# Optimization experiments

Measured on AMD Instinct MI355X. Metric: run time of the kernel, lower is better.

## Reference

```python
import jax, jax.numpy as jnp
import numpy as np

B, C, H, W = 8, 512, 90, 160
CK = C // 8
OUT = 512


def setup_inputs() -> dict:
    key = jax.random.key(0)
    ks = jax.random.split(key, 10)
    s = 0.02
    return {
        "x": jax.random.normal(ks[0], (B, C, H, W), dtype=jnp.float32),
        "Wq": jax.random.normal(ks[1], (CK, C), dtype=jnp.float32) * s,
        "bq": jax.random.normal(ks[2], (CK,), dtype=jnp.float32) * s,
        "Wk": jax.random.normal(ks[3], (CK, C), dtype=jnp.float32) * s,
        "bk": jax.random.normal(ks[4], (CK,), dtype=jnp.float32) * s,
        "Wv": jax.random.normal(ks[5], (C, C), dtype=jnp.float32) * s,
        "bv": jax.random.normal(ks[6], (C,), dtype=jnp.float32) * s,
        "gamma": jax.random.normal(ks[7], (1,), dtype=jnp.float32) * s,
        "Wo": jax.random.normal(ks[8], (OUT, C), dtype=jnp.float32) * s,
        "bo": jax.random.normal(ks[9], (OUT,), dtype=jnp.float32) * s,
    }


def reference(x, Wq, bq, Wk, bk, Wv, bv, gamma, Wo, bo):
    b, c, h, w = x.shape
    n = h * w
    xf = x.reshape(b, c, n)                                   # [B,C,N]
    # 1x1 convs == channel matmuls
    q = jnp.einsum('kc,bcn->bkn', Wq, xf) + bq[None, :, None]  # [B,CK,N]
    k = jnp.einsum('kc,bcn->bkn', Wk, xf) + bk[None, :, None]  # [B,CK,N]
    v = jnp.einsum('oc,bcn->bon', Wv, xf) + bv[None, :, None]  # [B,C,N]
    k = jax.nn.softmax(k, axis=2)   # softmax over spatial
    q = jax.nn.softmax(q, axis=1)   # softmax over channel
    # linear attention: small [CK,C] context, never an NxN map
    context = jnp.einsum('bkn,bcn->bkc', k, v)                 # [B,CK,C]
    out = jnp.einsum('bkc,bkn->bcn', context, q)               # [B,C,N]
    out = gamma[0] * out + xf
    out = jnp.einsum('oc,bcn->bon', Wo, out) + bo[None, :, None]
    return out.reshape(b, -1, h, w)
```

## Files before the change

### kernel.cpp

```cpp
#include <hip/hip_runtime.h>
#include <math.h>

#define NSP   14400
#define CCH   512
#define CKC   64
#define BSZ   8
#define OUTC  512

typedef unsigned short u16;
typedef unsigned int   u32;
typedef __attribute__((ext_vector_type(8))) short bf16x8;
typedef __attribute__((ext_vector_type(4))) float f32x4;

__device__ __forceinline__ u16 f2b(float f) {
    u32 u = __float_as_uint(f);
    return (u16)((u + 0x7fffu + ((u >> 16) & 1u)) >> 16);
}
__device__ __forceinline__ float b2f(u16 h) {
    return __uint_as_float(((u32)h) << 16);
}

__global__ __launch_bounds__(256) void prep_w(
    const float* __restrict__ Wq, const float* __restrict__ Wk,
    const float* __restrict__ Wo, const float* __restrict__ bq,
    const float* __restrict__ bk,
    u16* __restrict__ wqk, u16* __restrict__ wo_bf, float* __restrict__ bqk)
{
    int idx = blockIdx.x * 256 + threadIdx.x;
    if (idx < 128 * 512) {
        int r = idx >> 9, c = idx & 511;
        float v = (r < 64) ? Wq[r * 512 + c] : Wk[(r - 64) * 512 + c];
        wqk[idx] = f2b(v);
    } else if (idx < 128 * 512 + 512 * 512) {
        int i = idx - 128 * 512;
        wo_bf[i] = f2b(Wo[i]);
    } else if (idx < 128 * 512 + 512 * 512 + 128) {
        int i = idx - (128 * 512 + 512 * 512);
        bqk[i] = (i < 64) ? bq[i] : bk[i - 64];
    }
}

__global__ __launch_bounds__(256) void wov_gemm(
    const float* __restrict__ A, const float* __restrict__ B, float* __restrict__ Cg)
{
    const int t = threadIdx.x;
    const int n0 = blockIdx.x * 64, m0 = blockIdx.y * 64;
    __shared__ float As[16][68], Bs[16][68];
    const int ti = t >> 4, tj = t & 15;
    const int a_kk = t & 15, a_mm = t >> 4;
    const int b_nn = t & 63, b_kk = t >> 6;
    float acc[4][4] = {};
    for (int k0 = 0; k0 < 512; k0 += 16) {
        #pragma unroll
        for (int r = 0; r < 4; ++r)
            As[a_kk][a_mm + r * 16] = A[(size_t)(m0 + a_mm + r * 16) * 512 + k0 + a_kk];
        #pragma unroll
        for (int r = 0; r < 4; ++r)
            Bs[b_kk + r * 4][b_nn] = B[(size_t)(k0 + b_kk + r * 4) * 512 + n0 + b_nn];
        __syncthreads();
        #pragma unroll
        for (int kk = 0; kk < 16; ++kk) {
            const float4 a4 = *(const float4*)&As[kk][ti * 4];
            const float4 b4 = *(const float4*)&Bs[kk][tj * 4];
            const float av[4] = {a4.x, a4.y, a4.z, a4.w};
            const float bv[4] = {b4.x, b4.y, b4.z, b4.w};
            #pragma unroll
            for (int i = 0; i < 4; ++i)
                #pragma unroll
                for (int j = 0; j < 4; ++j)
                    acc[i][j] = fmaf(av[i], bv[j], acc[i][j]);
        }
        __syncthreads();
    }
    #pragma unroll
    for (int i = 0; i < 4; ++i) {
        float4 o = {acc[i][0], acc[i][1], acc[i][2], acc[i][3]};
        *(float4*)&Cg[(size_t)(m0 + ti * 4 + i) * 512 + n0 + tj * 4] = o;
    }
}

__global__ __launch_bounds__(64) void bov_kernel(
    const float* __restrict__ Wo, const float* __restrict__ bv, float* __restrict__ bov)
{
    int o = blockIdx.x * 64 + threadIdx.x;
    float s = 0.f;
    for (int c = 0; c < 512; ++c) s += Wo[(size_t)o * 512 + c] * bv[c];
    bov[o] = s;
}

__global__ __launch_bounds__(256) void xpose_cvt(
    const float* __restrict__ x, u16* __restrict__ xT)
{
    const int b = blockIdx.z, c0 = blockIdx.y * 64, n0 = blockIdx.x * 64;
    const int t = threadIdx.x, w = t >> 6;
    __shared__ float T[64][65];
    const float* xp = x + ((size_t)b * CCH + c0) * NSP + n0;
    const int nn = t & 63;
    #pragma unroll
    for (int r = 0; r < 16; ++r) {
        int cc = r * 4 + w;
        T[cc][nn] = xp[(size_t)cc * NSP + nn];
    }
    __syncthreads();
    u16* op = xT + ((size_t)b * NSP + n0) * CCH + c0;
    const int cw = t & 63;
    #pragma unroll
    for (int r = 0; r < 16; ++r) {
        int nr = r * 4 + w;
        op[(size_t)nr * CCH + cw] = f2b(T[cw][nr]);
    }
}

template<int MODE>
__global__ __launch_bounds__(256) void gemm_mfma(
    const u16* __restrict__ A, int lda, long aBatch,
    const u16* __restrict__ Bm, int K, long bBatch,
    float* __restrict__ outF, u16* __restrict__ outH, long cBatch,
    const float* __restrict__ bias, const u16* __restrict__ Ybf, long yBatch)
{
    const int t = threadIdx.x, lane = t & 63, w = t >> 6;
    const int b  = blockIdx.z;
    const int m0 = blockIdx.x * 128;
    const int n0 = blockIdx.y * 96;
    const int wm = w >> 1, wn = w & 1;

    __shared__ __align__(16) u16 As[128 * 64];
    __shared__ __align__(16) u16 Bs[96 * 64];

    const u16* Ap = A + (size_t)b * aBatch;
    const u16* Bp = Bm + (size_t)b * bBatch;

    const int srow = lane >> 3;
    const int kus  = (lane & 7) * 8;

    f32x4 acc[4][3];
    #pragma unroll
    for (int i = 0; i < 4; ++i)
        #pragma unroll
        for (int j = 0; j < 3; ++j)
            acc[i][j] = (f32x4){0.f, 0.f, 0.f, 0.f};

    for (int k0 = 0; k0 < K; k0 += 64) {
        bf16x8 ar[4], br[3];
        #pragma unroll
        for (int i = 0; i < 4; ++i) {
            int row = (w * 4 + i) * 8 + srow;
            ar[i] = *(const bf16x8*)(Ap + (size_t)(m0 + row) * lda + k0 + kus);
        }
        #pragma unroll
        for (int i = 0; i < 3; ++i) {
            int row = (w * 3 + i) * 8 + srow;
            br[i] = *(const bf16x8*)(Bp + (size_t)(n0 + row) * K + k0 + kus);
        }
        __syncthreads();
        #pragma unroll
        for (int i = 0; i < 4; ++i) {
            int row = (w * 4 + i) * 8 + srow;
            *(bf16x8*)&As[row * 64 + (kus ^ ((row & 7) << 3))] = ar[i];
        }
        #pragma unroll
        for (int i = 0; i < 3; ++i) {
            int row = (w * 3 + i) * 8 + srow;
            *(bf16x8*)&Bs[row * 64 + (kus ^ ((row & 7) << 3))] = br[i];
        }
        __syncthreads();
        #pragma unroll
        for (int kk = 0; kk < 2; ++kk) {
            const int kf = kk * 32 + (lane >> 4) * 8;
            bf16x8 af[4], bg[3];
            #pragma unroll
            for (int fm = 0; fm < 4; ++fm) {
                int ml = wm * 64 + fm * 16 + (lane & 15);
                af[fm] = *(const bf16x8*)&As[ml * 64 + (kf ^ ((ml & 7) << 3))];
            }
            #pragma unroll
            for (int fn = 0; fn < 3; ++fn) {
                int nl = wn * 48 + fn * 16 + (lane & 15);
                bg[fn] = *(const bf16x8*)&Bs[nl * 64 + (kf ^ ((nl & 7) << 3))];
            }
            #pragma unroll
            for (int fm = 0; fm < 4; ++fm)
                #pragma unroll
                for (int fn = 0; fn < 3; ++fn)
                    acc[fm][fn] = __builtin_amdgcn_mfma_f32_16x16x32_bf16(
                        af[fm], bg[fn], acc[fm][fn], 0, 0, 0);
        }
    }

    const int rbase = (lane >> 4) * 4;
    const int cloc  = lane & 15;
    #pragma unroll
    for (int fm = 0; fm < 4; ++fm) {
        #pragma unroll
        for (int fn = 0; fn < 3; ++fn) {
            const int gm0 = m0 + wm * 64 + fm * 16 + rbase;
            const int gn  = n0 + wn * 48 + fn * 16 + cloc;
            #pragma unroll
            for (int r = 0; r < 4; ++r) {
                const int gm = gm0 + r;
                const float v = acc[fm][fn][r];
                const size_t idx = (size_t)b * cBatch + (size_t)gm * NSP + gn;
                if (MODE == 0)      outF[idx] = v + bias[gm];
                else if (MODE == 1) outH[idx] = f2b(v + bias[gm]);
                else                outF[idx] = v + b2f(Ybf[(size_t)b * yBatch + (size_t)gm * NSP + gn]);
            }
        }
    }
}

__global__ __launch_bounds__(256) void k_stats(
    const float* __restrict__ Oqk, float* __restrict__ kmax, float* __restrict__ kinv)
{
    const int row = blockIdx.x;
    const int b = row >> 6, k = row & 63;
    const float4* p4 = (const float4*)(Oqk + ((size_t)b * 128 + 64 + k) * NSP);
    const int t = threadIdx.x;

    float m = -1e30f;
    for (int i = t; i < NSP / 4; i += 256) {
        float4 v = p4[i];
        m = fmaxf(m, fmaxf(fmaxf(v.x, v.y), fmaxf(v.z, v.w)));
    }
    for (int o = 32; o; o >>= 1) m = fmaxf(m, __shfl_xor(m, o));
    __shared__ float redm[4];
    const int wid = t >> 6, lane = t & 63;
    if (lane == 0) redm[wid] = m;
    __syncthreads();
    m = fmaxf(fmaxf(redm[0], redm[1]), fmaxf(redm[2], redm[3]));

    float s = 0.f;
    for (int i = t; i < NSP / 4; i += 256) {
        float4 v = p4[i];
        s += __expf(v.x - m) + __expf(v.y - m) + __expf(v.z - m) + __expf(v.w - m);
    }
    for (int o = 32; o; o >>= 1) s += __shfl_xor(s, o);
    __shared__ float reds[4];
    if (lane == 0) reds[wid] = s;
    __syncthreads();
    s = reds[0] + reds[1] + reds[2] + reds[3];
    if (t == 0) { kmax[row] = m; kinv[row] = 1.0f / s; }
}

__global__ __launch_bounds__(256) void q_softmax(
    const float* __restrict__ Oqk, u16* __restrict__ qT)
{
    const long idx = (long)blockIdx.x * 256 + threadIdx.x;
    const int b = (int)(idx / NSP);
    const int n = (int)(idx % NSP);
    const float* base = Oqk + (size_t)b * 128 * NSP + n;
    float q[64];
    float m = -1e30f;
    #pragma unroll
    for (int k = 0; k < 64; ++k) { q[k] = base[(size_t)k * NSP]; m = fmaxf(m, q[k]); }
    float s = 0.f;
    #pragma unroll
    for (int k = 0; k < 64; ++k) { q[k] = __expf(q[k] - m); s += q[k]; }
    const float inv = 1.0f / s;
    u32 pk[32];
    #pragma unroll
    for (int i = 0; i < 32; ++i) {
        pk[i] = (u32)f2b(q[2 * i] * inv) | ((u32)f2b(q[2 * i + 1] * inv) << 16);
    }
    uint4* dst = (uint4*)(qT + ((size_t)b * NSP + n) * 64);
    const uint4* src = (const uint4*)pk;
    #pragma unroll
    for (int i = 0; i < 8; ++i) dst[i] = src[i];
}

__global__ __launch_bounds__(256) void kx_partial(
    const float* __restrict__ Oqk, const float* __restrict__ x,
    const float* __restrict__ kmax, const float* __restrict__ kinv,
    float* __restrict__ part)
{
    const int c0 = blockIdx.x * 64;
    const int sp = blockIdx.y;
    const int b  = blockIdx.z;
    const int t  = threadIdx.x;
    const int ti = t >> 4, tj = t & 15;
    __shared__ float Ks[16][68];
    __shared__ float Vs[16][68];
    const int l_nn = t & 15, l_r0 = t >> 4;
    const float* kbase = Oqk + ((size_t)b * 128 + 64) * NSP;
    const float* xbase = x + (size_t)b * CCH * NSP;

    float km[4], ki[4];
    #pragma unroll
    for (int r = 0; r < 4; ++r) {
        int k = l_r0 + r * 16;
        km[r] = kmax[b * 64 + k];
        ki[r] = kinv[b * 64 + k];
    }
    float acc[4][4] = {};
    const int ns = sp * 960;
    for (int n0 = ns; n0 < ns + 960; n0 += 16) {
        #pragma unroll
        for (int r = 0; r < 4; ++r) {
            int kc = l_r0 + r * 16;
            Ks[l_nn][kc] = __expf(kbase[(size_t)kc * NSP + n0 + l_nn] - km[r]) * ki[r];
            Vs[l_nn][kc] = xbase[(size_t)(c0 + kc) * NSP + n0 + l_nn];
        }
        __syncthreads();
        #pragma unroll
        for (int nn = 0; nn < 16; ++nn) {
            const float4 a4 = *(const float4*)&Ks[nn][ti * 4];
            const float4 b4 = *(const float4*)&Vs[nn][tj * 4];
            const float av[4] = {a4.x, a4.y, a4.z, a4.w};
            const float bv[4] = {b4.x, b4.y, b4.z, b4.w};
            #pragma unroll
            for (int i = 0; i < 4; ++i)
                #pragma unroll
                for (int j = 0; j < 4; ++j)
                    acc[i][j] = fmaf(av[i], bv[j], acc[i][j]);
        }
        __syncthreads();
    }
    #pragma unroll
    for (int i = 0; i < 4; ++i) {
        float4 o = {acc[i][0], acc[i][1], acc[i][2], acc[i][3]};
        *(float4*)&part[(size_t)sp * (BSZ * 64 * 512) +
                        ((size_t)b * 64 + ti * 4 + i) * 512 + c0 + tj * 4] = o;
    }
}

__global__ __launch_bounds__(256) void kx_reduce(
    const float* __restrict__ part, float* __restrict__ KXf)
{
    const size_t idx = (size_t)blockIdx.x * 256 + threadIdx.x;
    float s = 0.f;
    #pragma unroll
    for (int sp = 0; sp < 15; ++sp) s += part[(size_t)sp * 262144 + idx];
    KXf[idx] = s;
}

__global__ __launch_bounds__(256) void wco_gemm(
    const float* __restrict__ Wov, const float* __restrict__ KXf,
    const float* __restrict__ bov, const float* __restrict__ gamma,
    u16* __restrict__ Wco)
{
    const int t = threadIdx.x;
    const int n0 = blockIdx.x * 64, m0 = blockIdx.y * 64;
    __shared__ float As[16][68], Bs[16][68];
    const int ti = t >> 4, tj = t & 15;
    const int a_kk = t & 15, a_mm = t >> 4;
    const int s_nn = t & 63, s_kq = t >> 6;
    float acc[4][4] = {};
    for (int k0 = 0; k0 < 512; k0 += 16) {
        #pragma unroll
        for (int r = 0; r < 4; ++r)
            As[a_kk][a_mm + r * 16] = Wov[(size_t)(m0 + a_mm + r * 16) * 512 + k0 + a_kk];
        {
            const float4 v = *(const float4*)&KXf[(size_t)(n0 + s_nn) * 512 + k0 + s_kq * 4];
            Bs[s_kq * 4 + 0][s_nn] = v.x;
            Bs[s_kq * 4 + 1][s_nn] = v.y;
            Bs[s_kq * 4 + 2][s_nn] = v.z;
            Bs[s_kq * 4 + 3][s_nn] = v.w;
        }
        __syncthreads();
        #pragma unroll
        for (int kk = 0; kk < 16; ++kk) {
            const float4 a4 = *(const float4*)&As[kk][ti * 4];
            const float4 b4 = *(const float4*)&Bs[kk][tj * 4];
            const float av[4] = {a4.x, a4.y, a4.z, a4.w};
            const float bv[4] = {b4.x, b4.y, b4.z, b4.w};
            #pragma unroll
            for (int i = 0; i < 4; ++i)
                #pragma unroll
                for (int j = 0; j < 4; ++j)
                    acc[i][j] = fmaf(av[i], bv[j], acc[i][j]);
        }
        __syncthreads();
    }
    const float g = gamma[0];
    #pragma unroll
    for (int i = 0; i < 4; ++i) {
        const int m = m0 + ti * 4 + i;
        const float bb = bov[m];
        #pragma unroll
        for (int j = 0; j < 4; ++j)
            Wco[(size_t)m * 512 + n0 + tj * 4 + j] = f2b(g * (acc[i][j] + bb));
    }
}

extern "C" void kernel_launch(void* const* d_in, const int* in_sizes, int n_in,
                              void* d_out, int out_size, void* d_ws, size_t ws_size,
                              hipStream_t stream)
{
    const float* x     = (const float*)d_in[0];
    const float* Wq    = (const float*)d_in[1];
    const float* bq    = (const float*)d_in[2];
    const float* Wk    = (const float*)d_in[3];
    const float* bk    = (const float*)d_in[4];
    const float* Wv    = (const float*)d_in[5];
    const float* bv    = (const float*)d_in[6];
    const float* gamma = (const float*)d_in[7];
    const float* Wo    = (const float*)d_in[8];
    const float* bo    = (const float*)d_in[9];
    float* out = (float*)d_out;

    char* base = (char*)d_ws;
    size_t off = 0;
    auto carve = [&](size_t bytes) { char* p = base + off; off = (off + bytes + 255) & ~(size_t)255; return p; };
    u16*   wqk   = (u16*)  carve(128 * 512 * 2);
    u16*   wo_bf = (u16*)  carve(512 * 512 * 2);
    float* bqk   = (float*)carve(128 * 4);
    float* Wov   = (float*)carve(512 * 512 * 4);
    float* bovp  = (float*)carve(512 * 4);
    u16*   xT    = (u16*)  carve((size_t)BSZ * NSP * CCH * 2);
    float* Oqk   = (float*)carve((size_t)BSZ * 128 * NSP * 4);
    u16*   Ybf   = (u16*)  carve((size_t)BSZ * 512 * NSP * 2);
    float* kmax  = (float*)carve(512 * 4);
    float* kinv  = (float*)carve(512 * 4);
    u16*   qT    = (u16*)  carve((size_t)BSZ * NSP * 64 * 2);
    float* part  = (float*)carve((size_t)15 * BSZ * 64 * 512 * 4);
    float* KXf   = (float*)carve((size_t)BSZ * 64 * 512 * 4);
    u16*   Wco   = (u16*)  carve(512 * 512 * 2);

    prep_w<<<dim3((128 * 512 + 512 * 512 + 128 + 255) / 256), dim3(256), 0, stream>>>(
        Wq, Wk, Wo, bq, bk, wqk, wo_bf, bqk);
    wov_gemm<<<dim3(8, 8), dim3(256), 0, stream>>>(Wo, Wv, Wov);
    bov_kernel<<<dim3(8), dim3(64), 0, stream>>>(Wo, bv, bovp);
    xpose_cvt<<<dim3(NSP / 64, CCH / 64, BSZ), dim3(256), 0, stream>>>(x, xT);
    gemm_mfma<0><<<dim3(1, NSP / 96, BSZ), dim3(256), 0, stream>>>(
        wqk, 512, 0L, xT, 512, (long)NSP * 512,
        Oqk, (u16*)nullptr, (long)128 * NSP, bqk, (const u16*)nullptr, 0L);
    gemm_mfma<1><<<dim3(4, NSP / 96, BSZ), dim3(256), 0, stream>>>(
        wo_bf, 512, 0L, xT, 512, (long)NSP * 512,
        (float*)nullptr, Ybf, (long)512 * NSP, bo, (const u16*)nullptr, 0L);
    k_stats<<<dim3(BSZ * 64), dim3(256), 0, stream>>>(Oqk, kmax, kinv);
    q_softmax<<<dim3(BSZ * NSP / 256), dim3(256), 0, stream>>>(Oqk, qT);
    kx_partial<<<dim3(CCH / 64, 15, BSZ), dim3(256), 0, stream>>>(Oqk, x, kmax, kinv, part);
    kx_reduce<<<dim3(262144 / 256), dim3(256), 0, stream>>>(part, KXf);
    wco_gemm<<<dim3(8, 8), dim3(256), 0, stream>>>(Wov, KXf, bovp, gamma, Wco);
    gemm_mfma<2><<<dim3(4, NSP / 96, BSZ), dim3(256), 0, stream>>>(
        Wco, 512, 64L, qT, 64, (long)NSP * 64,
        out, (u16*)nullptr, (long)512 * NSP, (const float*)nullptr, Ybf, (long)512 * NSP);
}
```

Baseline: 858.6 us.

## Fuse q-softmax into QK GEMM, use MFMA for KX, merge output GEMMs

After: 705.4 us. -17.8%, faster.

```diff
diff --git a/kernel.cpp b/kernel.cpp
--- a/kernel.cpp
+++ b/kernel.cpp
@@ -3,9 +3,7 @@
 
 #define NSP   14400
 #define CCH   512
-#define CKC   64
 #define BSZ   8
-#define OUTC  512
 
 typedef unsigned short u16;
 typedef unsigned int   u32;
@@ -15,9 +13,6 @@
 __device__ __forceinline__ u16 f2b(float f) {
     u32 u = __float_as_uint(f);
     return (u16)((u + 0x7fffu + ((u >> 16) & 1u)) >> 16);
-}
-__device__ __forceinline__ float b2f(u16 h) {
-    return __uint_as_float(((u32)h) << 16);
 }
 
 __global__ __launch_bounds__(256) void prep_w(
@@ -89,17 +84,20 @@
 }
 
 __global__ __launch_bounds__(256) void xpose_cvt(
-    const float* __restrict__ x, u16* __restrict__ xT)
+    const float* __restrict__ x, u16* __restrict__ xT, u16* __restrict__ xbf)
 {
     const int b = blockIdx.z, c0 = blockIdx.y * 64, n0 = blockIdx.x * 64;
     const int t = threadIdx.x, w = t >> 6;
     __shared__ float T[64][65];
     const float* xp = x + ((size_t)b * CCH + c0) * NSP + n0;
+    u16* op2 = xbf + ((size_t)b * CCH + c0) * NSP + n0;
     const int nn = t & 63;
     #pragma unroll
     for (int r = 0; r < 16; ++r) {
         int cc = r * 4 + w;
-        T[cc][nn] = xp[(size_t)cc * NSP + nn];
+        float v = xp[(size_t)cc * NSP + nn];
+        T[cc][nn] = v;
+        op2[(size_t)cc * NSP + nn] = f2b(v);
     }
     __syncthreads();
     u16* op = xT + ((size_t)b * NSP + n0) * CCH + c0;
@@ -111,25 +109,20 @@
     }
 }
 
-template<int MODE>
-__global__ __launch_bounds__(256) void gemm_mfma(
-    const u16* __restrict__ A, int lda, long aBatch,
-    const u16* __restrict__ Bm, int K, long bBatch,
-    float* __restrict__ outF, u16* __restrict__ outH, long cBatch,
-    const float* __restrict__ bias, const u16* __restrict__ Ybf, long yBatch)
+__global__ __launch_bounds__(256) void qk_gemm(
+    const u16* __restrict__ wqk, const u16* __restrict__ xT,
+    const float* __restrict__ bqk,
+    float* __restrict__ Okk, u16* __restrict__ qT)
 {
     const int t = threadIdx.x, lane = t & 63, w = t >> 6;
     const int b  = blockIdx.z;
-    const int m0 = blockIdx.x * 128;
-    const int n0 = blockIdx.y * 96;
+    const int n0 = blockIdx.x * 96;
     const int wm = w >> 1, wn = w & 1;
 
     __shared__ __align__(16) u16 As[128 * 64];
     __shared__ __align__(16) u16 Bs[96 * 64];
 
-    const u16* Ap = A + (size_t)b * aBatch;
-    const u16* Bp = Bm + (size_t)b * bBatch;
-
+    const u16* Bp = xT + (size_t)b * NSP * 512;
     const int srow = lane >> 3;
     const int kus  = (lane & 7) * 8;
 
@@ -140,17 +133,17 @@
         for (int j = 0; j < 3; ++j)
             acc[i][j] = (f32x4){0.f, 0.f, 0.f, 0.f};
 
-    for (int k0 = 0; k0 < K; k0 += 64) {
+    for (int k0 = 0; k0 < 512; k0 += 64) {
         bf16x8 ar[4], br[3];
         #pragma unroll
         for (int i = 0; i < 4; ++i) {
             int row = (w * 4 + i) * 8 + srow;
-            ar[i] = *(const bf16x8*)(Ap + (size_t)(m0 + row) * lda + k0 + kus);
+            ar[i] = *(const bf16x8*)(wqk + (size_t)row * 512 + k0 + kus);
         }
         #pragma unroll
         for (int i = 0; i < 3; ++i) {
             int row = (w * 3 + i) * 8 + srow;
-            br[i] = *(const bf16x8*)(Bp + (size_t)(n0 + row) * K + k0 + kus);
+            br[i] = *(const bf16x8*)(Bp + (size_t)(n0 + row) * 512 + k0 + kus);
         }
         __syncthreads();
         #pragma unroll
@@ -189,31 +182,64 @@
 
     const int rbase = (lane >> 4) * 4;
     const int cloc  = lane & 15;
-    #pragma unroll
-    for (int fm = 0; fm < 4; ++fm) {
+    if (wm == 0) {
         #pragma unroll
         for (int fn = 0; fn < 3; ++fn) {
-            const int gm0 = m0 + wm * 64 + fm * 16 + rbase;
-            const int gn  = n0 + wn * 48 + fn * 16 + cloc;
-            #pragma unroll
-            for (int r = 0; r < 4; ++r) {
-                const int gm = gm0 + r;
-                const float v = acc[fm][fn][r];
-                const size_t idx = (size_t)b * cBatch + (size_t)gm * NSP + gn;
-                if (MODE == 0)      outF[idx] = v + bias[gm];
-                else if (MODE == 1) outH[idx] = f2b(v + bias[gm]);
-                else                outF[idx] = v + b2f(Ybf[(size_t)b * yBatch + (size_t)gm * NSP + gn]);
+            const int gn = n0 + wn * 48 + fn * 16 + cloc;
+            float v[4][4];
+            float mx = -1e30f;
+            #pragma unroll
+            for (int fm = 0; fm < 4; ++fm)
+                #pragma unroll
+                for (int r = 0; r < 4; ++r) {
+                    v[fm][r] = acc[fm][fn][r] + bqk[fm * 16 + rbase + r];
+                    mx = fmaxf(mx, v[fm][r]);
+                }
+            mx = fmaxf(mx, __shfl_xor(mx, 16));
+            mx = fmaxf(mx, __shfl_xor(mx, 32));
+            float s = 0.f;
+            #pragma unroll
+            for (int fm = 0; fm < 4; ++fm)
+                #pragma unroll
+                for (int r = 0; r < 4; ++r) {
+                    v[fm][r] = __expf(v[fm][r] - mx);
+                    s += v[fm][r];
+                }
+            s += __shfl_xor(s, 16);
+            s += __shfl_xor(s, 32);
+            const float inv = 1.0f / s;
+            u16* qrow = qT + ((size_t)b * NSP + gn) * 64;
+            #pragma unroll
+            for (int fm = 0; fm < 4; ++fm) {
+                ushort4 pk;
+                pk.x = f2b(v[fm][0] * inv);
+                pk.y = f2b(v[fm][1] * inv);
+                pk.z = f2b(v[fm][2] * inv);
+                pk.w = f2b(v[fm][3] * inv);
+                *(ushort4*)&qrow[fm * 16 + rbase] = pk;
+            }
+        }
+    } else {
+        #pragma unroll
+        for (int fm = 0; fm < 4; ++fm) {
+            #pragma unroll
+            for (int fn = 0; fn < 3; ++fn) {
+                const int gn = n0 + wn * 48 + fn * 16 + cloc;
+                #pragma unroll
+                for (int r = 0; r < 4; ++r) {
+                    const int gmk = fm * 16 + rbase + r;
+                    Okk[((size_t)b * 64 + gmk) * NSP + gn] = acc[fm][fn][r] + bqk[64 + gmk];
+                }
             }
         }
     }
 }
 
 __global__ __launch_bounds__(256) void k_stats(
-    const float* __restrict__ Oqk, float* __restrict__ kmax, float* __restrict__ kinv)
+    const float* __restrict__ Okk, float* __restrict__ kmax, float* __restrict__ kinv)
 {
     const int row = blockIdx.x;
-    const int b = row >> 6, k = row & 63;
-    const float4* p4 = (const float4*)(Oqk + ((size_t)b * 128 + 64 + k) * NSP);
+    const float4* p4 = (const float4*)(Okk + (size_t)row * NSP);
     const int t = threadIdx.x;
 
     float m = -1e30f;
@@ -241,85 +267,108 @@
     if (t == 0) { kmax[row] = m; kinv[row] = 1.0f / s; }
 }
 
-__global__ __launch_bounds__(256) void q_softmax(
-    const float* __restrict__ Oqk, u16* __restrict__ qT)
-{
-    const long idx = (long)blockIdx.x * 256 + threadIdx.x;
-    const int b = (int)(idx / NSP);
-    const int n = (int)(idx % NSP);
-    const float* base = Oqk + (size_t)b * 128 * NSP + n;
-    float q[64];
-    float m = -1e30f;
-    #pragma unroll
-    for (int k = 0; k < 64; ++k) { q[k] = base[(size_t)k * NSP]; m = fmaxf(m, q[k]); }
-    float s = 0.f;
-    #pragma unroll
-    for (int k = 0; k < 64; ++k) { q[k] = __expf(q[k] - m); s += q[k]; }
-    const float inv = 1.0f / s;
-    u32 pk[32];
-    #pragma unroll
-    for (int i = 0; i < 32; ++i) {
-        pk[i] = (u32)f2b(q[2 * i] * inv) | ((u32)f2b(q[2 * i + 1] * inv) << 16);
-    }
-    uint4* dst = (uint4*)(qT + ((size_t)b * NSP + n) * 64);
-    const uint4* src = (const uint4*)pk;
-    #pragma unroll
-    for (int i = 0; i < 8; ++i) dst[i] = src[i];
-}
-
-__global__ __launch_bounds__(256) void kx_partial(
-    const float* __restrict__ Oqk, const float* __restrict__ x,
+__global__ __launch_bounds__(256) void kx_mfma(
+    const float* __restrict__ Okk, const u16* __restrict__ xbf,
     const float* __restrict__ kmax, const float* __restrict__ kinv,
     float* __restrict__ part)
 {
-    const int c0 = blockIdx.x * 64;
-    const int sp = blockIdx.y;
-    const int b  = blockIdx.z;
-    const int t  = threadIdx.x;
-    const int ti = t >> 4, tj = t & 15;
-    __shared__ float Ks[16][68];
-    __shared__ float Vs[16][68];
-    const int l_nn = t & 15, l_r0 = t >> 4;
-    const float* kbase = Oqk + ((size_t)b * 128 + 64) * NSP;
-    const float* xbase = x + (size_t)b * CCH * NSP;
-
-    float km[4], ki[4];
-    #pragma unroll
-    for (int r = 0; r < 4; ++r) {
-        int k = l_r0 + r * 16;
-        km[r] = kmax[b * 64 + k];
-        ki[r] = kinv[b * 64 + k];
-    }
-    float acc[4][4] = {};
-    const int ns = sp * 960;
-    for (int n0 = ns; n0 < ns + 960; n0 += 16) {
-        #pragma unroll
-        for (int r = 0; r < 4; ++r) {
-            int kc = l_r0 + r * 16;
-            Ks[l_nn][kc] = __expf(kbase[(size_t)kc * NSP + n0 + l_nn] - km[r]) * ki[r];
-            Vs[l_nn][kc] = xbase[(size_t)(c0 + kc) * NSP + n0 + l_nn];
-        }
-        __syncthreads();
-        #pragma unroll
-        for (int nn = 0; nn < 16; ++nn) {
-            const float4 a4 = *(const float4*)&Ks[nn][ti * 4];
-            const float4 b4 = *(const float4*)&Vs[nn][tj * 4];
-            const float av[4] = {a4.x, a4.y, a4.z, a4.w};
-            const float bv[4] = {b4.x, b4.y, b4.z, b4.w};
-            #pragma unroll
-            for (int i = 0; i < 4; ++i)
-                #pragma unroll
-                for (int j = 0; j < 4; ++j)
-                    acc[i][j] = fmaf(av[i], bv[j], acc[i][j]);
-        }
-        __syncthreads();
-    }
-    #pragma unroll
-    for (int i = 0; i < 4; ++i) {
-        float4 o = {acc[i][0], acc[i][1], acc[i][2], acc[i][3]};
-        *(float4*)&part[(size_t)sp * (BSZ * 64 * 512) +
-                        ((size_t)b * 64 + ti * 4 + i) * 512 + c0 + tj * 4] = o;
-    }
+    const int bid = blockIdx.x;
+    const int swz = (bid & 7) * 100 + (bid >> 3);
+    const int c_t = swz & 3;
+    const int tmp = swz >> 2;
+    const int sp  = tmp % 25;
+    const int b   = tmp / 25;
+    const int c0  = c_t * 128;
+    const int t = threadIdx.x, lane = t & 63, w = t >> 6;
+
+    __shared__ __align__(16) u16 As[64 * 64];
+    __shared__ __align__(16) u16 Bs[128 * 64];
+    __shared__ float kms[64], kis[64];
+    if (t < 64) { kms[t] = kmax[b * 64 + t]; kis[t] = kinv[b * 64 + t]; }
+    __syncthreads();
+
+    const float* kb = Okk + (size_t)b * 64 * NSP;
+    const u16*   xb = xbf + ((size_t)b * CCH + c0) * NSP;
+
+    const int arow = t >> 4;
+    const int acol = (t & 15) * 4;
+    const int brow = t >> 3;
+    const int bgr  = (t & 7) * 8;
+
+    f32x4 acc[4][2];
+    #pragma unroll
+    for (int i = 0; i < 4; ++i)
+        #pragma unroll
+        for (int j = 0; j < 2; ++j)
+            acc[i][j] = (f32x4){0.f, 0.f, 0.f, 0.f};
+
+    const int ns = sp * 576;
+    for (int nb = ns; nb < ns + 576; nb += 64) {
+        float4 av[4];
+        bf16x8 bv[4];
+        #pragma unroll
+        for (int p = 0; p < 4; ++p) {
+            int row = arow + p * 16;
+            av[p] = *(const float4*)&kb[(size_t)row * NSP + nb + acol];
+        }
+        #pragma unroll
+        for (int p = 0; p < 4; ++p) {
+            int row = brow + p * 32;
+            bv[p] = *(const bf16x8*)&xb[(size_t)row * NSP + nb + bgr];
+        }
+        __syncthreads();
+        #pragma unroll
+        for (int p = 0; p < 4; ++p) {
+            int row = arow + p * 16;
+            float km = kms[row], ki = kis[row];
+            ushort4 e;
+            e.x = f2b(__expf(av[p].x - km) * ki);
+            e.y = f2b(__expf(av[p].y - km) * ki);
+            e.z = f2b(__expf(av[p].z - km) * ki);
+            e.w = f2b(__expf(av[p].w - km) * ki);
+            *(ushort4*)&As[row * 64 + (acol ^ ((row & 7) << 3))] = e;
+        }
+        #pragma unroll
+        for (int p = 0; p < 4; ++p) {
+            int row = brow + p * 32;
+            *(bf16x8*)&Bs[row * 64 + (bgr ^ ((row & 7) << 3))] = bv[p];
+        }
+        __syncthreads();
+        #pragma unroll
+        for (int kk = 0; kk < 2; ++kk) {
+            const int kf = kk * 32 + (lane >> 4) * 8;
+            bf16x8 af[4], bg[2];
+            #pragma unroll
+            for (int fm = 0; fm < 4; ++fm) {
+                int ml = fm * 16 + (lane & 15);
+                af[fm] = *(const bf16x8*)&As[ml * 64 + (kf ^ ((ml & 7) << 3))];
+            }
+            #pragma unroll
+            for (int fn = 0; fn < 2; ++fn) {
+                int nl = w * 32 + fn * 16 + (lane & 15);
+                bg[fn] = *(const bf16x8*)&Bs[nl * 64 + (kf ^ ((nl & 7) << 3))];
+            }
+            #pragma unroll
+            for (int fm = 0; fm < 4; ++fm)
+                #pragma unroll
+                for (int fn = 0; fn < 2; ++fn)
+                    acc[fm][fn] = __builtin_amdgcn_mfma_f32_16x16x32_bf16(
+                        af[fm], bg[fn], acc[fm][fn], 0, 0, 0);
+        }
+    }
+
+    const int rbase = (lane >> 4) * 4;
+    const int cloc  = lane & 15;
+    #pragma unroll
+    for (int fm = 0; fm < 4; ++fm)
+        #pragma unroll
+        for (int fn = 0; fn < 2; ++fn)
+            #pragma unroll
+            for (int r = 0; r < 4; ++r) {
+                const int k = fm * 16 + rbase + r;
+                const int c = c0 + w * 32 + fn * 16 + cloc;
+                part[(((size_t)sp * 8 + b) * 64 + k) * 512 + c] = acc[fm][fn][r];
+            }
 }
 
 __global__ __launch_bounds__(256) void kx_reduce(
@@ -328,7 +377,7 @@
     const size_t idx = (size_t)blockIdx.x * 256 + threadIdx.x;
     float s = 0.f;
     #pragma unroll
-    for (int sp = 0; sp < 15; ++sp) s += part[(size_t)sp * 262144 + idx];
+    for (int sp = 0; sp < 25; ++sp) s += part[(size_t)sp * 262144 + idx];
     KXf[idx] = s;
 }
 
@@ -378,6 +427,110 @@
         #pragma unroll
         for (int j = 0; j < 4; ++j)
             Wco[(size_t)m * 512 + n0 + tj * 4 + j] = f2b(g * (acc[i][j] + bb));
+    }
+}
+
+__global__ __launch_bounds__(256) void fused_out(
+    const u16* __restrict__ Wco, const u16* __restrict__ wo_bf,
+    const u16* __restrict__ qT, const u16* __restrict__ xT,
+    const float* __restrict__ bo, float* __restrict__ out)
+{
+    const int bid = blockIdx.x;
+    const int swz = (bid & 7) * 600 + (bid >> 3);
+    const int m_t = swz & 3;
+    const int tmp = swz >> 2;
+    const int n_t = tmp % 150;
+    const int b   = tmp / 150;
+    const int m0 = m_t * 128, n0 = n_t * 96;
+    const int t = threadIdx.x, lane = t & 63, w = t >> 6;
+    const int wm = w >> 1, wn = w & 1;
+
+    __shared__ __align__(16) u16 As[128 * 64];
+    __shared__ __align__(16) u16 Bs[96 * 64];
+
+    const int srow = lane >> 3;
+    const int kus  = (lane & 7) * 8;
+
+    f32x4 acc[4][3];
+    #pragma unroll
+    for (int i = 0; i < 4; ++i)
+        #pragma unroll
+        for (int j = 0; j < 3; ++j)
+            acc[i][j] = (f32x4){0.f, 0.f, 0.f, 0.f};
+
+    for (int k0 = 0; k0 < 576; k0 += 64) {
+        bf16x8 ar[4], br[3];
+        if (k0 == 0) {
+            #pragma unroll
+            for (int i = 0; i < 4; ++i) {
+                int row = (w * 4 + i) * 8 + srow;
+                ar[i] = *(const bf16x8*)(Wco + (size_t)(m0 + row) * 512 + b * 64 + kus);
+            }
+            #pragma unroll
+            for (int i = 0; i < 3; ++i) {
+                int row = (w * 3 + i) * 8 + srow;
+                br[i] = *(const bf16x8*)(qT + ((size_t)b * NSP + n0 + row) * 64 + kus);
+            }
+        } else {
+            const int kc = k0 - 64;
+            #pragma unroll
+            for (int i = 0; i < 4; ++i) {
+                int row = (w * 4 + i) * 8 + srow;
+                ar[i] = *(const bf16x8*)(wo_bf + (size_t)(m0 + row) * 512 + kc + kus);
+            }
+            #pragma unroll
+            for (int i = 0; i < 3; ++i) {
+                int row = (w * 3 + i) * 8 + srow;
+                br[i] = *(const bf16x8*)(xT + ((size_t)b * NSP + n0 + row) * 512 + kc + kus);
+            }
+        }
+        __syncthreads();
+        #pragma unroll
+        for (int i = 0; i < 4; ++i) {
+            int row = (w * 4 + i) * 8 + srow;
+            *(bf16x8*)&As[row * 64 + (kus ^ ((row & 7) << 3))] = ar[i];
+        }
+        #pragma unroll
+        for (int i = 0; i < 3; ++i) {
+            int row = (w * 3 + i) * 8 + srow;
+            *(bf16x8*)&Bs[row * 64 + (kus ^ ((row & 7) << 3))] = br[i];
+        }
+        __syncthreads();
+        #pragma unroll
+        for (int kk = 0; kk < 2; ++kk) {
+            const int kf = kk * 32 + (lane >> 4) * 8;
+            bf16x8 af[4], bg[3];
+            #pragma unroll
+            for (int fm = 0; fm < 4; ++fm) {
+                int ml = wm * 64 + fm * 16 + (lane & 15);
+                af[fm] = *(const bf16x8*)&As[ml * 64 + (kf ^ ((ml & 7) << 3))];
+            }
+            #pragma unroll
+            for (int fn = 0; fn < 3; ++fn) {
+                int nl = wn * 48 + fn * 16 + (lane & 15);
+                bg[fn] = *(const bf16x8*)&Bs[nl * 64 + (kf ^ ((nl & 7) << 3))];
+            }
+            #pragma unroll
+            for (int fm = 0; fm < 4; ++fm)
+                #pragma unroll
+                for (int fn = 0; fn < 3; ++fn)
+                    acc[fm][fn] = __builtin_amdgcn_mfma_f32_16x16x32_bf16(
+                        af[fm], bg[fn], acc[fm][fn], 0, 0, 0);
+        }
+    }
+
+    const int rbase = (lane >> 4) * 4;
+    const int cloc  = lane & 15;
+    #pragma unroll
+    for (int fm = 0; fm < 4; ++fm) {
+        #pragma unroll
+        for (int fn = 0; fn < 3; ++fn) {
+            const int gm = m0 + wm * 64 + fm * 16 + rbase;
+            const int gn = n0 + wn * 48 + fn * 16 + cloc;
+            #pragma unroll
+            for (int r = 0; r < 4; ++r)
+                out[((size_t)b * 512 + gm + r) * NSP + gn] = acc[fm][fn][r] + bo[gm + r];
+        }
     }
 }
 
@@ -406,12 +559,12 @@
     float* Wov   = (float*)carve(512 * 512 * 4);
     float* bovp  = (float*)carve(512 * 4);
     u16*   xT    = (u16*)  carve((size_t)BSZ * NSP * CCH * 2);
-    float* Oqk   = (float*)carve((size_t)BSZ * 128 * NSP * 4);
-    u16*   Ybf   = (u16*)  carve((size_t)BSZ * 512 * NSP * 2);
+    u16*   xbf   = (u16*)  carve((size_t)BSZ * CCH * NSP * 2);
+    float* Okk   = (float*)carve((size_t)BSZ * 64 * NSP * 4);
     float* kmax  = (float*)carve(512 * 4);
     float* kinv  = (float*)carve(512 * 4);
     u16*   qT    = (u16*)  carve((size_t)BSZ * NSP * 64 * 2);
-    float* part  = (float*)carve((size_t)15 * BSZ * 64 * 512 * 4);
+    float* part  = (float*)carve((size_t)25 * BSZ * 64 * 512 * 4);
     float* KXf   = (float*)carve((size_t)BSZ * 64 * 512 * 4);
     u16*   Wco   = (u16*)  carve(512 * 512 * 2);
 
@@ -419,19 +572,11 @@
         Wq, Wk, Wo, bq, bk, wqk, wo_bf, bqk);
     wov_gemm<<<dim3(8, 8), dim3(256), 0, stream>>>(Wo, Wv, Wov);
     bov_kernel<<<dim3(8), dim3(64), 0, stream>>>(Wo, bv, bovp);
-    xpose_cvt<<<dim3(NSP / 64, CCH / 64, BSZ), dim3(256), 0, stream>>>(x, xT);
-    gemm_mfma<0><<<dim3(1, NSP / 96, BSZ), dim3(256), 0, stream>>>(
-        wqk, 512, 0L, xT, 512, (long)NSP * 512,
-        Oqk, (u16*)nullptr, (long)128 * NSP, bqk, (const u16*)nullptr, 0L);
-    gemm_mfma<1><<<dim3(4, NSP / 96, BSZ), dim3(256), 0, stream>>>(
-        wo_bf, 512, 0L, xT, 512, (long)NSP * 512,
-        (float*)nullptr, Ybf, (long)512 * NSP, bo, (const u16*)nullptr, 0L);
-    k_stats<<<dim3(BSZ * 64), dim3(256), 0, stream>>>(Oqk, kmax, kinv);
-    q_softmax<<<dim3(BSZ * NSP / 256), dim3(256), 0, stream>>>(Oqk, qT);
-    kx_partial<<<dim3(CCH / 64, 15, BSZ), dim3(256), 0, stream>>>(Oqk, x, kmax, kinv, part);
+    xpose_cvt<<<dim3(NSP / 64, CCH / 64, BSZ), dim3(256), 0, stream>>>(x, xT, xbf);
+    qk_gemm<<<dim3(NSP / 96, 1, BSZ), dim3(256), 0, stream>>>(wqk, xT, bqk, Okk, qT);
+    k_stats<<<dim3(BSZ * 64), dim3(256), 0, stream>>>(Okk, kmax, kinv);
+    kx_mfma<<<dim3(4 * 25 * BSZ), dim3(256), 0, stream>>>(Okk, xbf, kmax, kinv, part);
     kx_reduce<<<dim3(262144 / 256), dim3(256), 0, stream>>>(part, KXf);
     wco_gemm<<<dim3(8, 8), dim3(256), 0, stream>>>(Wov, KXf, bovp, gamma, Wco);
-    gemm_mfma<2><<<dim3(4, NSP / 96, BSZ), dim3(256), 0, stream>>>(
-        Wco, 512, 64L, qT, 64, (long)NSP * 64,
-        out, (u16*)nullptr, (long)512 * NSP, (const float*)nullptr, Ybf, (long)512 * NSP);
-}
+    fused_out<<<dim3(4 * 150 * BSZ), dim3(256), 0, stream>>>(Wco, wo_bf, qT, xT, bo, out);
+}
```
